# Kernel tuning notes

Hardware: AMD Instinct MI355X
Metric: run time of the kernel (lower is better)

## Reference

```python
import jax, jax.numpy as jnp
import numpy as np

N, E, D = 50000, 800000, 128
BN_EPS = 1e-5
COORDS_WEIGHT = 1.0


def _p(key, shape, scale=0.05):
    return (jax.random.normal(key, shape, dtype=jnp.float32) * scale)


def setup_inputs() -> dict:
    key = jax.random.key(0)
    ks = jax.random.split(key, 16)
    inp = {
        "h": jax.random.normal(ks[0], (N, D), dtype=jnp.float32),
        "coord": jax.random.normal(ks[1], (N, 3), dtype=jnp.float32),
        "edge_index": jax.random.randint(ks[2], (2, E), 0, N, dtype=jnp.int32),
        # edge_mlp: Linear(2D+1 -> D), BN, ReLU, Linear(D -> D), BN, ReLU
        "e_w1": _p(ks[3], (D, 2 * D + 1)), "e_b1": jnp.zeros((D,), jnp.float32),
        "e_g1": jnp.ones((D,), jnp.float32), "e_be1": jnp.zeros((D,), jnp.float32),
        "e_w2": _p(ks[4], (D, D)), "e_b2": jnp.zeros((D,), jnp.float32),
        "e_g2": jnp.ones((D,), jnp.float32), "e_be2": jnp.zeros((D,), jnp.float32),
        # node_mlp: Linear(D + D -> D), BN, ReLU, Linear(D -> D)
        "n_w1": _p(ks[5], (D, 2 * D)), "n_b1": jnp.zeros((D,), jnp.float32),
        "n_g1": jnp.ones((D,), jnp.float32), "n_be1": jnp.zeros((D,), jnp.float32),
        "n_w2": _p(ks[6], (D, D)), "n_b2": jnp.zeros((D,), jnp.float32),
        # coord_mlp: Linear(D -> D), BN, ReLU, Linear(D -> 1, bias=False, tiny init)
        "c_w1": _p(ks[7], (D, D)), "c_b1": jnp.zeros((D,), jnp.float32),
        "c_g1": jnp.ones((D,), jnp.float32), "c_be1": jnp.zeros((D,), jnp.float32),
        "c_w2": _p(ks[8], (1, D), scale=0.001),
    }
    return inp


def _bn(x, g, b):
    # BatchNorm1d in training mode: biased batch stats over dim 0
    m = jnp.mean(x, axis=0)
    v = jnp.var(x, axis=0)
    return (x - m) * jax.lax.rsqrt(v + BN_EPS) * g + b


def _segment_mean(data, seg, num_segments):
    s = jax.ops.segment_sum(data, seg, num_segments=num_segments)
    c = jax.ops.segment_sum(jnp.ones((data.shape[0], 1), data.dtype), seg,
                            num_segments=num_segments)
    return s / jnp.maximum(c, 1.0)


def reference(h, coord, edge_index,
              e_w1, e_b1, e_g1, e_be1, e_w2, e_b2, e_g2, e_be2,
              n_w1, n_b1, n_g1, n_be1, n_w2, n_b2,
              c_w1, c_b1, c_g1, c_be1, c_w2):
    row, col = edge_index[0], edge_index[1]
    # coord2radial
    coord_diff = coord[row] - coord[col]                      # [E,3]
    radial = jnp.sum(coord_diff ** 2, axis=1, keepdims=True)  # [E,1]
    # edge_model
    e_in = jnp.concatenate([h[row], h[col], radial], axis=1)  # [E, 2D+1]
    x = jax.nn.relu(_bn(e_in @ e_w1.T + e_b1, e_g1, e_be1))
    edge_feat = jax.nn.relu(_bn(x @ e_w2.T + e_b2, e_g2, e_be2))  # [E,D]
    # coord_model
    y = jax.nn.relu(_bn(edge_feat @ c_w1.T + c_b1, c_g1, c_be1))
    scale = y @ c_w2.T                                        # [E,1]
    trans = jnp.clip(coord_diff * scale, -100.0, 100.0)
    coord_out = coord + _segment_mean(trans, row, coord.shape[0]) * COORDS_WEIGHT
    # node_model
    agg = _segment_mean(edge_feat, row, h.shape[0])           # [N,D]
    n_in = jnp.concatenate([h, agg], axis=1)                  # [N,2D]
    z = jax.nn.relu(_bn(n_in @ n_w1.T + n_b1, n_g1, n_be1))
    h_out = h + (z @ n_w2.T + n_b2)                           # recurrent residual
    return (h_out, coord_out)
```

## Files before the change

### kernel.cpp

```cpp
#include <hip/hip_runtime.h>

#define Nn 50000
#define En 800000
#define NSLOT 64
#define MGRID 384

typedef __attribute__((ext_vector_type(8))) short short8;
typedef __attribute__((ext_vector_type(4))) float f32x4;

union U8 { uint4 u4; unsigned short us[8]; unsigned int ui[4]; short8 s8; };

static __device__ __forceinline__ float bf2f(unsigned int lo16) {
  return __uint_as_float(lo16 << 16);
}
static __device__ __forceinline__ unsigned short f2bf(float f) {
  unsigned int x = __float_as_uint(f);
  return (unsigned short)((x + 0x7FFFu + ((x >> 16) & 1u)) >> 16);
}
static __device__ __forceinline__ unsigned int f2bf2(float a, float b) {
  unsigned int r;
  asm("v_cvt_pk_bf16_f32 %0, %1, %2" : "=v"(r) : "v"(a), "v"(b));
  return r;
}


__global__ __launch_bounds__(256) void k_prep_h(const float* __restrict__ h,
                                                unsigned short* __restrict__ nodeA) {
  int idx = blockIdx.x * 256 + threadIdx.x;
  if (idx >= Nn * 128) return;
  int n = idx >> 7, k = idx & 127;
  nodeA[(size_t)n * 256 + k] = f2bf(h[idx]);
}

__global__ __launch_bounds__(256) void k_prep_w(const float* __restrict__ src,
                                                unsigned short* __restrict__ dst, int Ksrc,
                                                int koff, int kshift, int total) {
  int idx = blockIdx.x * 256 + threadIdx.x;
  if (idx >= total) return;
  int n = idx >> kshift;
  int k = idx & ((1 << kshift) - 1);
  dst[idx] = f2bf(src[n * Ksrc + koff + k]);
}

__global__ void k_wlast(const float* __restrict__ e_w1, float* __restrict__ wlast) {
  int t = threadIdx.x;
  if (t < 128) wlast[t] = e_w1[t * 257 + 256];
}


__global__ __launch_bounds__(256) void k_count(const int* __restrict__ row, int* __restrict__ cnt) {
  int e = blockIdx.x * 256 + threadIdx.x;
  atomicAdd(&cnt[row[e]], 1);
}

__global__ __launch_bounds__(256) void k_fill(const int* __restrict__ row,
                                              const int* __restrict__ col,
                                              int* __restrict__ cursor,
                                              unsigned short* __restrict__ rowS,
                                              unsigned short* __restrict__ colS) {
  int e = blockIdx.x * 256 + threadIdx.x;
  int r = row[e];
  int pos = atomicAdd(&cursor[r], 1);
  rowS[pos] = (unsigned short)r;
  colS[pos] = (unsigned short)col[e];
}

__global__ __launch_bounds__(1024) void k_scan(const int* __restrict__ cnt, int* __restrict__ start,
                                               int* __restrict__ cursor, int n) {
  __shared__ int wsum[16];
  __shared__ int carry;
  int tid = threadIdx.x, lane = tid & 63, wid = tid >> 6;
  if (tid == 0) carry = 0;
  __syncthreads();
  for (int base = 0; base < n; base += 1024) {
    int i = base + tid;
    int v = (i < n) ? cnt[i] : 0;
    int x = v;
#pragma unroll
    for (int d = 1; d < 64; d <<= 1) {
      int y = __shfl_up(x, d, 64);
      if (lane >= d) x += y;
    }
    if (lane == 63) wsum[wid] = x;
    __syncthreads();
    if (wid == 0) {
      int s = (lane < 16) ? wsum[lane] : 0;
#pragma unroll
      for (int d = 1; d < 16; d <<= 1) {
        int y = __shfl_up(s, d, 64);
        if (lane >= d) s += y;
      }
      if (lane < 16) wsum[lane] = s;
    }
    __syncthreads();
    int c0 = carry;
    int waveoff = (wid > 0) ? wsum[wid - 1] : 0;
    int incl = c0 + waveoff + x;
    if (i < n) {
      start[i] = incl - v;
      cursor[i] = incl - v;
    }
    __syncthreads();
    if (tid == 1023) carry = incl;
    __syncthreads();
  }
}


__global__ void k_fin(const float* __restrict__ statS, const float* __restrict__ statQ,
                      const float* __restrict__ g, const float* __restrict__ be, float invR,
                      float* __restrict__ bnS, float* __restrict__ bnSh) {
  int c = threadIdx.x;
  if (c >= 128) return;
  float s = 0.f, q = 0.f;
  for (int k = 0; k < NSLOT; ++k) {
    s += statS[k * 128 + c];
    q += statQ[k * 128 + c];
  }
  float mean = s * invR;
  float var = fmaxf(q * invR - mean * mean, 0.f);
  float rs = rsqrtf(var + 1e-5f);
  float sc = g[c] * rs;
  bnS[c] = sc;
  bnSh[c] = be[c] - mean * sc;
}

template <int KSTEPS, bool BN_A, bool STATS, bool FP32OUT, bool STORE>
__global__ __launch_bounds__(256) void k_gemmW(
    const unsigned short* __restrict__ A, int Astride,
    const unsigned short* __restrict__ W, const float* __restrict__ bias,
    const float* __restrict__ bnS, const float* __restrict__ bnSh,
    unsigned short* __restrict__ outb, float* __restrict__ statS, float* __restrict__ statQ,
    const float* __restrict__ hres, float* __restrict__ outf, int R) {
  constexpr int K = KSTEPS * 32;
  constexpr int WST = K + 8;
  constexpr int SEGS = K / 8;
  __shared__ __align__(16) unsigned short smem[128 * WST];
  __shared__ float ssum[4][128], ssq[4][128];
  int tid = threadIdx.x;
  int w = tid >> 6, lane = tid & 63, m = lane & 15, kq = lane >> 4;
  int rbase = blockIdx.x * 128;
#pragma unroll
  for (int it = 0; it < SEGS / 2; ++it) {
    int idx = it * 256 + tid;
    int n = idx / SEGS, seg = idx % SEGS;
    uint4 v = *(const uint4*)(W + (size_t)n * K + seg * 8);
    *(uint4*)(smem + n * WST + seg * 8) = v;
  }
  __syncthreads();
  int row0 = rbase + w * 32 + m;
  int rc0 = min(row0, R - 1);
  int rc1 = min(row0 + 16, R - 1);
  f32x4 acc[2][8];
#pragma unroll
  for (int rt = 0; rt < 2; ++rt)
#pragma unroll
    for (int c = 0; c < 8; ++c) acc[rt][c] = (f32x4){0.f, 0.f, 0.f, 0.f};
#pragma unroll
  for (int ks = 0; ks < KSTEPS; ++ks) {
    int k0 = ks * 32 + kq * 8;
    U8 ua0, ua1;
    ua0.u4 = *(const uint4*)(A + (size_t)rc0 * Astride + k0);
    ua1.u4 = *(const uint4*)(A + (size_t)rc1 * Astride + k0);
    if (BN_A) {
      const float4* sp = (const float4*)(bnS + k0);
      const float4* hp = (const float4*)(bnSh + k0);
      float4 s0 = sp[0], s1 = sp[1], h0 = hp[0], h1 = hp[1];
      float sv[8] = {s0.x, s0.y, s0.z, s0.w, s1.x, s1.y, s1.z, s1.w};
      float hv[8] = {h0.x, h0.y, h0.z, h0.w, h1.x, h1.y, h1.z, h1.w};
      U8 pa, pb;
#pragma unroll
      for (int jj = 0; jj < 4; ++jj) {
        float a0 = fmaxf(bf2f(ua0.us[2 * jj]) * sv[2 * jj] + hv[2 * jj], 0.f);
        float a1 = fmaxf(bf2f(ua0.us[2 * jj + 1]) * sv[2 * jj + 1] + hv[2 * jj + 1], 0.f);
        float b0 = fmaxf(bf2f(ua1.us[2 * jj]) * sv[2 * jj] + hv[2 * jj], 0.f);
        float b1 = fmaxf(bf2f(ua1.us[2 * jj + 1]) * sv[2 * jj + 1] + hv[2 * jj + 1], 0.f);
        pa.ui[jj] = f2bf2(a0, a1);
        pb.ui[jj] = f2bf2(b0, b1);
      }
      ua0 = pa;
      ua1 = pb;
    }
#pragma unroll
    for (int c = 0; c < 8; ++c) {
      U8 ub;
      ub.u4 = *(const uint4*)(smem + (c * 16 + m) * WST + k0);
      acc[0][c] = __builtin_amdgcn_mfma_f32_16x16x32_bf16(ua0.s8, ub.s8, acc[0][c], 0, 0, 0);
      acc[1][c] = __builtin_amdgcn_mfma_f32_16x16x32_bf16(ua1.s8, ub.s8, acc[1][c], 0, 0, 0);
    }
  }
  if constexpr (FP32OUT) {
#pragma unroll
    for (int rt = 0; rt < 2; ++rt)
#pragma unroll
      for (int c = 0; c < 8; ++c) {
        int n = c * 16 + m;
        float bn_ = bias[n];
#pragma unroll
        for (int j = 0; j < 4; ++j) {
          int rr = rbase + w * 32 + rt * 16 + kq * 4 + j;
          if (rr < R) {
            size_t o = (size_t)rr * 128 + n;
            outf[o] = acc[rt][c][j] + bn_ + hres[o];
          }
        }
      }
  } else {
    if constexpr (STORE) __syncthreads();
    unsigned short* tile = smem;
#pragma unroll
    for (int c = 0; c < 8; ++c) {
      int n = c * 16 + m;
      float bn_ = bias ? bias[n] : 0.f;
      float s = 0.f, q = 0.f;
#pragma unroll
      for (int rt = 0; rt < 2; ++rt)
#pragma unroll
        for (int j = 0; j < 4; ++j) {
          int lr = w * 32 + rt * 16 + kq * 4 + j;
          float v = acc[rt][c][j] + bn_;
          if (STORE) tile[lr * 136 + n] = f2bf(v);
          if (STATS) {
            float sv = (rbase + lr < R) ? v : 0.f;
            s += sv;
            q = fmaf(sv, sv, q);
          }
        }
      if (STATS) {
        s += __shfl_xor(s, 16, 64); s += __shfl_xor(s, 32, 64);
        q += __shfl_xor(q, 16, 64); q += __shfl_xor(q, 32, 64);
        if (kq == 0) { ssum[w][n] = s; ssq[w][n] = q; }
      }
    }
    if constexpr (STORE) {
      __syncthreads();
      const uint4* tl = (const uint4*)tile;
#pragma unroll
      for (int u = 0; u < 8; ++u) {
        int idx = u * 256 + tid;
        int rr = idx >> 4, seg = idx & 15;
        if (rbase + rr < R)
          *(uint4*)(outb + (size_t)(rbase + rr) * 128 + seg * 8) = tl[rr * 17 + seg];
      }
    }
    if (STATS) {
      __syncthreads();
      if (tid < 128) {
        float s = ssum[0][tid] + ssum[1][tid] + ssum[2][tid] + ssum[3][tid];
        float q = ssq[0][tid] + ssq[1][tid] + ssq[2][tid] + ssq[3][tid];
        int slot = blockIdx.x & (NSLOT - 1);
        atomicAdd(&statS[slot * 128 + tid], s);
        atomicAdd(&statQ[slot * 128 + tid], q);
      }
    }
  }
}

__global__ __launch_bounds__(256) void k_stats1(
    const unsigned short* __restrict__ hWr, const unsigned short* __restrict__ hWc,
    const float* __restrict__ coord, const unsigned short* __restrict__ rowS,
    const unsigned short* __restrict__ colS, const float* __restrict__ wlast,
    float* __restrict__ radS, float* __restrict__ statS, float* __restrict__ statQ,
    int per_wave) {
  int tid = threadIdx.x, lane = tid & 63;
  int wid = blockIdx.x * 4 + (tid >> 6);
  int e0 = wid * per_wave;
  int e1 = min(e0 + per_wave, En);
  int c2 = lane * 2;
  float wl0 = wlast[c2], wl1 = wlast[c2 + 1];
  float s0 = 0.f, s1 = 0.f, q0 = 0.f, q1 = 0.f;
  for (int e = e0; e < e1; e += 2) {
    int ra = rowS[e], ca = colS[e];
    int rb = rowS[e + 1], cb = colS[e + 1];
    float ax = coord[ra * 3 + 0] - coord[ca * 3 + 0];
    float ay = coord[ra * 3 + 1] - coord[ca * 3 + 1];
    float az = coord[ra * 3 + 2] - coord[ca * 3 + 2];
    float bx = coord[rb * 3 + 0] - coord[cb * 3 + 0];
    float by = coord[rb * 3 + 1] - coord[cb * 3 + 1];
    float bz = coord[rb * 3 + 2] - coord[cb * 3 + 2];
    float rada = ax * ax + ay * ay + az * az;
    float radb = bx * bx + by * by + bz * bz;
    if (lane == 0) {
      radS[e] = rada;
      radS[e + 1] = radb;
    }
    unsigned int uar = *(const unsigned int*)(hWr + (size_t)ra * 128 + c2);
    unsigned int uac = *(const unsigned int*)(hWc + (size_t)ca * 128 + c2);
    unsigned int ubr = *(const unsigned int*)(hWr + (size_t)rb * 128 + c2);
    unsigned int ubc = *(const unsigned int*)(hWc + (size_t)cb * 128 + c2);
    float va0 = bf2f(uar & 0xFFFFu) + bf2f(uac & 0xFFFFu) + rada * wl0;
    float va1 = bf2f(uar >> 16) + bf2f(uac >> 16) + rada * wl1;
    float vb0 = bf2f(ubr & 0xFFFFu) + bf2f(ubc & 0xFFFFu) + radb * wl0;
    float vb1 = bf2f(ubr >> 16) + bf2f(ubc >> 16) + radb * wl1;
    s0 += va0 + vb0;
    s1 += va1 + vb1;
    q0 = fmaf(va0, va0, q0); q0 = fmaf(vb0, vb0, q0);
    q1 = fmaf(va1, va1, q1); q1 = fmaf(vb1, vb1, q1);
  }
  int slot = wid & (NSLOT - 1);
  atomicAdd(&statS[slot * 128 + c2], s0);
  atomicAdd(&statS[slot * 128 + c2 + 1], s1);
  atomicAdd(&statQ[slot * 128 + c2], q0);
  atomicAdd(&statQ[slot * 128 + c2 + 1], q1);
}

__global__ __launch_bounds__(256) void k_egemm2(
    const unsigned short* __restrict__ hWr, const unsigned short* __restrict__ hWc,
    const float* __restrict__ radS, const unsigned short* __restrict__ rowS,
    const unsigned short* __restrict__ colS, const unsigned short* __restrict__ W,
    const float* __restrict__ bias, const float* __restrict__ wlast,
    const float* __restrict__ bnS1, const float* __restrict__ bnSh1,
    unsigned short* __restrict__ outb, float* __restrict__ statS, float* __restrict__ statQ) {
  constexpr int WST = 136;
  __shared__ __align__(16) unsigned short smem[128 * WST];
  __shared__ float ssum[4][128], ssq[4][128];
  int tid = threadIdx.x;
  int w = tid >> 6, lane = tid & 63, m = lane & 15, kq = lane >> 4;
  int rbase = blockIdx.x * 128;
#pragma unroll
  for (int it = 0; it < 8; ++it) {
    int idx = it * 256 + tid;
    int n = idx >> 4, seg = idx & 15;
    uint4 v = *(const uint4*)(W + (size_t)n * 128 + seg * 8);
    *(uint4*)(smem + n * WST + seg * 8) = v;
  }
  int rc0 = rbase + w * 32 + m, rc1 = rc0 + 16;
  int r0 = rowS[rc0], c0 = colS[rc0];
  int r1 = rowS[rc1], c1 = colS[rc1];
  float rad0 = radS[rc0], rad1 = radS[rc1];
  __syncthreads();
  f32x4 acc[2][8];
#pragma unroll
  for (int rt = 0; rt < 2; ++rt)
#pragma unroll
    for (int c = 0; c < 8; ++c) acc[rt][c] = (f32x4){0.f, 0.f, 0.f, 0.f};
#pragma unroll
  for (int ks = 0; ks < 4; ++ks) {
    int k0 = ks * 32 + kq * 8;
    U8 a0r, a0c, a1r, a1c;
    a0r.u4 = *(const uint4*)(hWr + (size_t)r0 * 128 + k0);
    a0c.u4 = *(const uint4*)(hWc + (size_t)c0 * 128 + k0);
    a1r.u4 = *(const uint4*)(hWr + (size_t)r1 * 128 + k0);
    a1c.u4 = *(const uint4*)(hWc + (size_t)c1 * 128 + k0);
    const float4* wp = (const float4*)(wlast + k0);
    const float4* sp = (const float4*)(bnS1 + k0);
    const float4* hp = (const float4*)(bnSh1 + k0);
    float4 w0 = wp[0], w1 = wp[1], sA = sp[0], sB = sp[1], hA = hp[0], hB = hp[1];
    float wv[8] = {w0.x, w0.y, w0.z, w0.w, w1.x, w1.y, w1.z, w1.w};
    float sv[8] = {sA.x, sA.y, sA.z, sA.w, sB.x, sB.y, sB.z, sB.w};
    float hv[8] = {hA.x, hA.y, hA.z, hA.w, hB.x, hB.y, hB.z, hB.w};
    U8 ua0, ua1;
#pragma unroll
    for (int jj = 0; jj < 4; ++jj) {
      int j0 = 2 * jj, j1 = 2 * jj + 1;
      float v0a = bf2f(a0r.us[j0]) + bf2f(a0c.us[j0]) + rad0 * wv[j0];
      float v0b = bf2f(a0r.us[j1]) + bf2f(a0c.us[j1]) + rad0 * wv[j1];
      float v1a = bf2f(a1r.us[j0]) + bf2f(a1c.us[j0]) + rad1 * wv[j0];
      float v1b = bf2f(a1r.us[j1]) + bf2f(a1c.us[j1]) + rad1 * wv[j1];
      v0a = fmaxf(v0a * sv[j0] + hv[j0], 0.f);
      v0b = fmaxf(v0b * sv[j1] + hv[j1], 0.f);
      v1a = fmaxf(v1a * sv[j0] + hv[j0], 0.f);
      v1b = fmaxf(v1b * sv[j1] + hv[j1], 0.f);
      ua0.ui[jj] = f2bf2(v0a, v0b);
      ua1.ui[jj] = f2bf2(v1a, v1b);
    }
#pragma unroll
    for (int c = 0; c < 8; ++c) {
      U8 ub;
      ub.u4 = *(const uint4*)(smem + (c * 16 + m) * WST + k0);
      acc[0][c] = __builtin_amdgcn_mfma_f32_16x16x32_bf16(ua0.s8, ub.s8, acc[0][c], 0, 0, 0);
      acc[1][c] = __builtin_amdgcn_mfma_f32_16x16x32_bf16(ua1.s8, ub.s8, acc[1][c], 0, 0, 0);
    }
  }
  __syncthreads();
  unsigned short* tile = smem;
#pragma unroll
  for (int c = 0; c < 8; ++c) {
    int n = c * 16 + m;
    float bn_ = bias[n];
    float s = 0.f, q = 0.f;
#pragma unroll
    for (int rt = 0; rt < 2; ++rt)
#pragma unroll
      for (int j = 0; j < 4; ++j) {
        int lr = w * 32 + rt * 16 + kq * 4 + j;
        float v = acc[rt][c][j] + bn_;
        tile[lr * 136 + n] = f2bf(v);
        s += v;
        q = fmaf(v, v, q);
      }
    s += __shfl_xor(s, 16, 64); s += __shfl_xor(s, 32, 64);
    q += __shfl_xor(q, 16, 64); q += __shfl_xor(q, 32, 64);
    if (kq == 0) { ssum[w][n] = s; ssq[w][n] = q; }
  }
  __syncthreads();
  const uint4* tl = (const uint4*)tile;
#pragma unroll
  for (int u = 0; u < 8; ++u) {
    int idx = u * 256 + tid;
    int rr = idx >> 4, seg = idx & 15;
    *(uint4*)(outb + (size_t)(rbase + rr) * 128 + seg * 8) = tl[rr * 17 + seg];
  }
  if (tid < 128) {
    float s = ssum[0][tid] + ssum[1][tid] + ssum[2][tid] + ssum[3][tid];
    float q = ssq[0][tid] + ssq[1][tid] + ssq[2][tid] + ssq[3][tid];
    int slot = blockIdx.x & (NSLOT - 1);
    atomicAdd(&statS[slot * 128 + tid], s);
    atomicAdd(&statQ[slot * 128 + tid], q);
  }
}

__global__ __launch_bounds__(256) void k_agg(const unsigned short* __restrict__ t,
                                             const int* __restrict__ start,
                                             const int* __restrict__ cnt,
                                             const float* __restrict__ bnS,
                                             const float* __restrict__ bnSh,
                                             unsigned short* __restrict__ nodeA) {
  int tid = threadIdx.x;
  int lane = tid & 63;
  int n = blockIdx.x * 4 + (tid >> 6);
  if (n >= Nn) return;
  int deg = cnt[n], off = start[n];
  int c2 = lane * 2;
  float s0 = bnS[c2], s1 = bnS[c2 + 1], h0 = bnSh[c2], h1 = bnSh[c2 + 1];
  float a0 = 0.f, a1 = 0.f;
  const unsigned short* p = t + (size_t)off * 128 + c2;
  for (int j = 0; j < deg; ++j) {
    unsigned int u = *(const unsigned int*)(p + (size_t)j * 128);
    a0 += fmaxf(bf2f(u & 0xFFFFu) * s0 + h0, 0.f);
    a1 += fmaxf(bf2f(u >> 16) * s1 + h1, 0.f);
  }
  float inv = 1.f / fmaxf((float)deg, 1.f);
  unsigned int o = (unsigned)f2bf(a0 * inv) | ((unsigned)f2bf(a1 * inv) << 16);
  *(unsigned int*)(nodeA + (size_t)n * 256 + 128 + c2) = o;
}

__global__ __launch_bounds__(256) void k_moment(
    const unsigned short* __restrict__ t,
    const float* __restrict__ bnS2, const float* __restrict__ bnSh2,
    float* __restrict__ Mpart, float* __restrict__ SyG) {
  constexpr int WST = 136;
  __shared__ __align__(16) unsigned short yT[128 * WST];
  __shared__ float s2L[128], h2L[128];
  int tid = threadIdx.x;
  int w = tid >> 6, lane = tid & 63, m = lane & 15, kq = lane >> 4;
  if (tid < 128) { s2L[tid] = bnS2[tid]; h2L[tid] = bnSh2[tid]; }
  f32x4 acc[2][8];
#pragma unroll
  for (int rt = 0; rt < 2; ++rt)
#pragma unroll
    for (int c = 0; c < 8; ++c) acc[rt][c] = (f32x4){0.f, 0.f, 0.f, 0.f};
  float sy[32];
#pragma unroll
  for (int i = 0; i < 32; ++i) sy[i] = 0.f;
  for (int tile = blockIdx.x; tile < En / 128; tile += MGRID) {
    __syncthreads();
    int e0 = tile * 128 + lane * 2;
    U8 ra[4], rb[4];
#pragma unroll
    for (int q = 0; q < 4; ++q) {
      ra[q].u4 = *(const uint4*)(t + (size_t)e0 * 128 + w * 32 + q * 8);
      rb[q].u4 = *(const uint4*)(t + (size_t)(e0 + 1) * 128 + w * 32 + q * 8);
    }
#pragma unroll
    for (int q = 0; q < 4; ++q)
#pragma unroll
      for (int i = 0; i < 8; ++i) {
        int c = w * 32 + q * 8 + i;
        float s = s2L[c], h = h2L[c];
        float ya = fmaxf(bf2f(ra[q].us[i]) * s + h, 0.f);
        float yb = fmaxf(bf2f(rb[q].us[i]) * s + h, 0.f);
        sy[q * 8 + i] += ya + yb;
        *(unsigned int*)(yT + c * WST + lane * 2) = f2bf2(ya, yb);
      }
    __syncthreads();
#pragma unroll
    for (int ks = 0; ks < 4; ++ks) {
      int k0 = ks * 32 + kq * 8;
      U8 a0, a1;
      a0.u4 = *(const uint4*)(yT + (w * 32 + m) * WST + k0);
      a1.u4 = *(const uint4*)(yT + (w * 32 + 16 + m) * WST + k0);
#pragma unroll
      for (int c = 0; c < 8; ++c) {
        U8 ub;
        ub.u4 = *(const uint4*)(yT + (c * 16 + m) * WST + k0);
        acc[0][c] = __builtin_amdgcn_mfma_f32_16x16x32_bf16(a0.s8, ub.s8, acc[0][c], 0, 0, 0);
        acc[1][c] = __builtin_amdgcn_mfma_f32_16x16x32_bf16(a1.s8, ub.s8, acc[1][c], 0, 0, 0);
      }
    }
  }
  size_t mb = (size_t)blockIdx.x * 16384;
#pragma unroll
  for (int rt = 0; rt < 2; ++rt)
#pragma unroll
    for (int c = 0; c < 8; ++c)
#pragma unroll
      for (int j = 0; j < 4; ++j)
        Mpart[mb + (size_t)(w * 32 + rt * 16 + kq * 4 + j) * 128 + c * 16 + m] = acc[rt][c][j];
#pragma unroll
  for (int i = 0; i < 32; ++i) {
    float s = sy[i];
#pragma unroll
    for (int d = 1; d < 64; d <<= 1) s += __shfl_xor(s, d, 64);
    if (lane == 0) atomicAdd(&SyG[w * 32 + i], s);
  }
}

__global__ __launch_bounds__(256) void k_msum(const float* __restrict__ Mpart,
                                              float* __restrict__ Mg) {
  __shared__ float red[4][64];
  int tid = threadIdx.x;
  int e = blockIdx.x * 64 + (tid & 63);
  int pq = tid >> 6;
  float s = 0.f;
  for (int k = pq * (MGRID / 4); k < (pq + 1) * (MGRID / 4); ++k)
    s += Mpart[(size_t)k * 16384 + e];
  red[pq][tid & 63] = s;
  __syncthreads();
  if (tid < 64) Mg[e] = red[0][tid] + red[1][tid] + red[2][tid] + red[3][tid];
}

__global__ __launch_bounds__(128) void k_fin3(
    const float* __restrict__ Mg, const float* __restrict__ Sy,
    const float* __restrict__ w1, const float* __restrict__ g,
    const float* __restrict__ be, float invE,
    float* __restrict__ bnS3, float* __restrict__ bnSh3) {
  __shared__ float sW[128];
  __shared__ float r2[4];
  int c = blockIdx.x, j = threadIdx.x;
  sW[j] = w1[c * 128 + j];
  __syncthreads();
  float a0 = 0.f, a1 = 0.f, a2 = 0.f, a3 = 0.f;
  for (int i = 0; i < 128; i += 4) {
    a0 = fmaf(sW[i], Mg[i * 128 + j], a0);
    a1 = fmaf(sW[i + 1], Mg[(i + 1) * 128 + j], a1);
    a2 = fmaf(sW[i + 2], Mg[(i + 2) * 128 + j], a2);
    a3 = fmaf(sW[i + 3], Mg[(i + 3) * 128 + j], a3);
  }
  float q = sW[j] * ((a0 + a1) + (a2 + a3));
  float dm = sW[j] * Sy[j];
#pragma unroll
  for (int d = 1; d < 64; d <<= 1) {
    q += __shfl_xor(q, d, 64);
    dm += __shfl_xor(dm, d, 64);
  }
  int wv = j >> 6;
  if ((j & 63) == 0) { r2[wv * 2] = q; r2[wv * 2 + 1] = dm; }
  __syncthreads();
  if (j == 0) {
    float quad = r2[0] + r2[2];
    float dmt = r2[1] + r2[3];
    float Eu = dmt * invE;
    float var = fmaxf(quad * invE - Eu * Eu, 0.f);
    float S = g[c] * rsqrtf(var + 1e-5f);
    bnS3[c] = S;
    bnSh3[c] = be[c] - Eu * S;
  }
}

__global__ __launch_bounds__(256) void k_cgemm(
    const unsigned short* __restrict__ A,
    const unsigned short* __restrict__ W,
    const float* __restrict__ bnS2, const float* __restrict__ bnSh2,
    const float* __restrict__ bnS3, const float* __restrict__ bnSh3,
    const float* __restrict__ cw2, float* __restrict__ scaleE) {
  constexpr int WST = 136;
  __shared__ __align__(16) unsigned short smem[128 * WST];
  int tid = threadIdx.x;
  int w = tid >> 6, lane = tid & 63, m = lane & 15, kq = lane >> 4;
  int rbase = blockIdx.x * 128;
#pragma unroll
  for (int it = 0; it < 8; ++it) {
    int idx = it * 256 + tid;
    int n = idx >> 4, seg = idx & 15;
    *(uint4*)(smem + n * WST + seg * 8) = *(const uint4*)(W + (size_t)n * 128 + seg * 8);
  }
  __syncthreads();
  int rc0 = rbase + w * 32 + m, rc1 = rc0 + 16;
  f32x4 acc[2][8];
#pragma unroll
  for (int rt = 0; rt < 2; ++rt)
#pragma unroll
    for (int c = 0; c < 8; ++c) acc[rt][c] = (f32x4){0.f, 0.f, 0.f, 0.f};
#pragma unroll
  for (int ks = 0; ks < 4; ++ks) {
    int k0 = ks * 32 + kq * 8;
    U8 ua0, ua1;
    ua0.u4 = *(const uint4*)(A + (size_t)rc0 * 128 + k0);
    ua1.u4 = *(const uint4*)(A + (size_t)rc1 * 128 + k0);
    const float4* sp = (const float4*)(bnS2 + k0);
    const float4* hp = (const float4*)(bnSh2 + k0);
    float4 s0 = sp[0], s1 = sp[1], h0 = hp[0], h1 = hp[1];
    float sv[8] = {s0.x, s0.y, s0.z, s0.w, s1.x, s1.y, s1.z, s1.w};
    float hv[8] = {h0.x, h0.y, h0.z, h0.w, h1.x, h1.y, h1.z, h1.w};
    U8 pa, pb;
#pragma unroll
    for (int jj = 0; jj < 4; ++jj) {
      float v0a = fmaxf(bf2f(ua0.us[2 * jj]) * sv[2 * jj] + hv[2 * jj], 0.f);
      float v0b = fmaxf(bf2f(ua0.us[2 * jj + 1]) * sv[2 * jj + 1] + hv[2 * jj + 1], 0.f);
      float v1a = fmaxf(bf2f(ua1.us[2 * jj]) * sv[2 * jj] + hv[2 * jj], 0.f);
      float v1b = fmaxf(bf2f(ua1.us[2 * jj + 1]) * sv[2 * jj + 1] + hv[2 * jj + 1], 0.f);
      pa.ui[jj] = f2bf2(v0a, v0b);
      pb.ui[jj] = f2bf2(v1a, v1b);
    }
#pragma unroll
    for (int c = 0; c < 8; ++c) {
      U8 ub;
      ub.u4 = *(const uint4*)(smem + (c * 16 + m) * WST + k0);
      acc[0][c] = __builtin_amdgcn_mfma_f32_16x16x32_bf16(pa.s8, ub.s8, acc[0][c], 0, 0, 0);
      acc[1][c] = __builtin_amdgcn_mfma_f32_16x16x32_bf16(pb.s8, ub.s8, acc[1][c], 0, 0, 0);
    }
  }
  float s3v[8], h3v[8], wv[8];
#pragma unroll
  for (int c = 0; c < 8; ++c) {
    int n = c * 16 + m;
    s3v[c] = bnS3[n];
    h3v[c] = bnSh3[n];
    wv[c] = cw2[n];
  }
  float p0[4] = {0.f, 0.f, 0.f, 0.f}, p1[4] = {0.f, 0.f, 0.f, 0.f};
#pragma unroll
  for (int c = 0; c < 8; ++c)
#pragma unroll
    for (int j = 0; j < 4; ++j) {
      p0[j] += fmaxf(acc[0][c][j] * s3v[c] + h3v[c], 0.f) * wv[c];
      p1[j] += fmaxf(acc[1][c][j] * s3v[c] + h3v[c], 0.f) * wv[c];
    }
#pragma unroll
  for (int j = 0; j < 4; ++j)
#pragma unroll
    for (int d = 1; d < 16; d <<= 1) {
      p0[j] += __shfl_xor(p0[j], d, 64);
      p1[j] += __shfl_xor(p1[j], d, 64);
    }
  if (m == 0) {
    int r0 = rbase + w * 32 + kq * 4;
    *(float4*)(scaleE + r0) = make_float4(p0[0], p0[1], p0[2], p0[3]);
    *(float4*)(scaleE + r0 + 16) = make_float4(p1[0], p1[1], p1[2], p1[3]);
  }
}

__global__ __launch_bounds__(256) void k_coord(const float* __restrict__ coord,
                                               const unsigned short* __restrict__ colS,
                                               const int* __restrict__ start,
                                               const int* __restrict__ cnt,
                                               const float* __restrict__ scaleE,
                                               float* __restrict__ cout) {
  int tid = threadIdx.x;
  int lane = tid & 63;
  int n = blockIdx.x * 4 + (tid >> 6);
  if (n >= Nn) return;
  int deg = cnt[n], off = start[n];
  float cx0 = coord[n * 3 + 0], cy0 = coord[n * 3 + 1], cz0 = coord[n * 3 + 2];
  float ax = 0.f, ay = 0.f, az = 0.f;
  for (int j = lane; j < deg; j += 64) {
    int e = off + j;
    int c = colS[e];
    float s = scaleE[e];
    float tx = (cx0 - coord[c * 3 + 0]) * s;
    float ty = (cy0 - coord[c * 3 + 1]) * s;
    float tz = (cz0 - coord[c * 3 + 2]) * s;
    ax += fminf(fmaxf(tx, -100.f), 100.f);
    ay += fminf(fmaxf(ty, -100.f), 100.f);
    az += fminf(fmaxf(tz, -100.f), 100.f);
  }
#pragma unroll
  for (int d = 32; d; d >>= 1) {
    ax += __shfl_xor(ax, d, 64);
    ay += __shfl_xor(ay, d, 64);
    az += __shfl_xor(az, d, 64);
  }
  if (lane == 0) {
    float inv = 1.f / fmaxf((float)deg, 1.f);
    cout[n * 3 + 0] = cx0 + ax * inv;
    cout[n * 3 + 1] = cy0 + ay * inv;
    cout[n * 3 + 2] = cz0 + az * inv;
  }
}


extern "C" void kernel_launch(void* const* d_in, const int* in_sizes, int n_in, void* d_out,
                              int out_size, void* d_ws, size_t ws_size, hipStream_t stream) {
  (void)in_sizes; (void)n_in; (void)out_size; (void)ws_size;
  const float* h = (const float*)d_in[0];
  const float* coord = (const float*)d_in[1];
  const int* eidx = (const int*)d_in[2];
  const int* row = eidx;
  const int* col = eidx + En;
  const float* e_w1 = (const float*)d_in[3];
  const float* e_b1 = (const float*)d_in[4];
  const float* e_g1 = (const float*)d_in[5];
  const float* e_be1 = (const float*)d_in[6];
  const float* e_w2 = (const float*)d_in[7];
  const float* e_b2 = (const float*)d_in[8];
  const float* e_g2 = (const float*)d_in[9];
  const float* e_be2 = (const float*)d_in[10];
  const float* n_w1 = (const float*)d_in[11];
  const float* n_b1 = (const float*)d_in[12];
  const float* n_g1 = (const float*)d_in[13];
  const float* n_be1 = (const float*)d_in[14];
  const float* n_w2 = (const float*)d_in[15];
  const float* n_b2 = (const float*)d_in[16];
  const float* c_w1 = (const float*)d_in[17];
  const float* c_b1 = (const float*)d_in[18];
  (void)c_b1;
  const float* c_g1 = (const float*)d_in[19];
  const float* c_be1 = (const float*)d_in[20];
  const float* c_w2 = (const float*)d_in[21];

  char* base = (char*)d_ws;
  size_t off = 0;
  auto alloc = [&](size_t bytes) -> void* {
    void* p = base + off;
    off = (off + bytes + 255) & ~(size_t)255;
    return p;
  };
  unsigned short* t = (unsigned short*)alloc((size_t)En * 128 * 2);
  unsigned short* nodeA = (unsigned short*)alloc((size_t)Nn * 256 * 2);
  unsigned short* hWr = (unsigned short*)alloc((size_t)Nn * 128 * 2);
  unsigned short* hWc = (unsigned short*)alloc((size_t)Nn * 128 * 2);
  float* scaleE = (float*)alloc((size_t)En * 4);
  float* radS = scaleE;
  unsigned short* rowS = (unsigned short*)alloc((size_t)En * 2);
  unsigned short* colS = (unsigned short*)alloc((size_t)En * 2);
  int* cnt = (int*)alloc((size_t)Nn * 4);
  int* startp = (int*)alloc((size_t)Nn * 4);
  int* cursor = (int*)alloc((size_t)Nn * 4);
  float* statS = (float*)alloc(4 * NSLOT * 128 * 4);
  float* statQ = (float*)alloc(4 * NSLOT * 128 * 4);
  float* bnS = (float*)alloc(4 * 128 * 4);
  float* bnSh = (float*)alloc(4 * 128 * 4);
  unsigned short* w1a = (unsigned short*)alloc(128 * 128 * 2);
  unsigned short* w1b = (unsigned short*)alloc(128 * 128 * 2);
  unsigned short* w2b = (unsigned short*)alloc(128 * 128 * 2);
  unsigned short* c1b = (unsigned short*)alloc(128 * 128 * 2);
  unsigned short* n1b = (unsigned short*)alloc(128 * 256 * 2);
  unsigned short* n2b = (unsigned short*)alloc(128 * 128 * 2);
  float* wlast = (float*)alloc(128 * 4);
  float* Mpart = (float*)hWr;
  float* Mg = scaleE;
  float* SyG = scaleE + 16384;

  hipMemsetAsync(cnt, 0, (size_t)Nn * 4, stream);
  hipMemsetAsync(statS, 0, 4 * NSLOT * 128 * 4, stream);
  hipMemsetAsync(statQ, 0, 4 * NSLOT * 128 * 4, stream);

  k_prep_h<<<(Nn * 128 + 255) / 256, 256, 0, stream>>>(h, nodeA);
  k_prep_w<<<(128 * 128 + 255) / 256, 256, 0, stream>>>(e_w1, w1a, 257, 0, 7, 128 * 128);
  k_prep_w<<<(128 * 128 + 255) / 256, 256, 0, stream>>>(e_w1, w1b, 257, 128, 7, 128 * 128);
  k_prep_w<<<(128 * 128 + 255) / 256, 256, 0, stream>>>(e_w2, w2b, 128, 0, 7, 128 * 128);
  k_prep_w<<<(128 * 128 + 255) / 256, 256, 0, stream>>>(c_w1, c1b, 128, 0, 7, 128 * 128);
  k_prep_w<<<(128 * 256 + 255) / 256, 256, 0, stream>>>(n_w1, n1b, 256, 0, 8, 128 * 256);
  k_prep_w<<<(128 * 128 + 255) / 256, 256, 0, stream>>>(n_w2, n2b, 128, 0, 7, 128 * 128);
  k_wlast<<<1, 128, 0, stream>>>(e_w1, wlast);

  k_count<<<En / 256, 256, 0, stream>>>(row, cnt);
  k_scan<<<1, 1024, 0, stream>>>(cnt, startp, cursor, Nn);
  k_fill<<<En / 256, 256, 0, stream>>>(row, col, cursor, rowS, colS);

  const int gridN = (Nn + 127) / 128;
  k_gemmW<4, false, false, false, true><<<gridN, 256, 0, stream>>>(
      nodeA, 256, w1a, e_b1, nullptr, nullptr, hWr, nullptr, nullptr, nullptr, nullptr, Nn);
  k_gemmW<4, false, false, false, true><<<gridN, 256, 0, stream>>>(
      nodeA, 256, w1b, nullptr, nullptr, nullptr, hWc, nullptr, nullptr, nullptr, nullptr, Nn);

  const int per_wave = ((En / 2 + 5119) / 5120) * 2;
  k_stats1<<<1280, 256, 0, stream>>>(hWr, hWc, coord, rowS, colS, wlast, radS,
                                     statS + 0 * NSLOT * 128, statQ + 0 * NSLOT * 128, per_wave);
  k_fin<<<1, 128, 0, stream>>>(statS + 0 * NSLOT * 128, statQ + 0 * NSLOT * 128, e_g1, e_be1,
                               1.f / En, bnS + 0, bnSh + 0);

  k_egemm2<<<En / 128, 256, 0, stream>>>(hWr, hWc, radS, rowS, colS, w2b, e_b2, wlast, bnS + 0,
                                         bnSh + 0, t, statS + 1 * NSLOT * 128,
                                         statQ + 1 * NSLOT * 128);
  k_fin<<<1, 128, 0, stream>>>(statS + 1 * NSLOT * 128, statQ + 1 * NSLOT * 128, e_g2, e_be2,
                               1.f / En, bnS + 128, bnSh + 128);

  k_agg<<<(Nn + 3) / 4, 256, 0, stream>>>(t, startp, cnt, bnS + 128, bnSh + 128, nodeA);

  hipMemsetAsync(SyG, 0, 128 * 4, stream);
  k_moment<<<MGRID, 256, 0, stream>>>(t, bnS + 128, bnSh + 128, Mpart, SyG);
  k_msum<<<256, 256, 0, stream>>>(Mpart, Mg);
  k_fin3<<<128, 128, 0, stream>>>(Mg, SyG, c_w1, c_g1, c_be1, 1.f / En, bnS + 256, bnSh + 256);

  k_cgemm<<<En / 128, 256, 0, stream>>>(t, c1b, bnS + 128, bnSh + 128, bnS + 256, bnSh + 256,
                                        c_w2, scaleE);

  float* hout = (float*)d_out;
  float* cout = hout + (size_t)Nn * 128;
  k_coord<<<(Nn + 3) / 4, 256, 0, stream>>>(coord, colS, startp, cnt, scaleE, cout);

  k_gemmW<8, false, true, false, true><<<gridN, 256, 0, stream>>>(
      nodeA, 256, n1b, n_b1, nullptr, nullptr, t, statS + 3 * NSLOT * 128,
      statQ + 3 * NSLOT * 128, nullptr, nullptr, Nn);
  k_fin<<<1, 128, 0, stream>>>(statS + 3 * NSLOT * 128, statQ + 3 * NSLOT * 128, n_g1, n_be1,
                               1.f / Nn, bnS + 384, bnSh + 384);
  k_gemmW<4, true, false, true, true><<<gridN, 256, 0, stream>>>(
      t, 128, n2b, n_b2, bnS + 384, bnSh + 384, nullptr, nullptr, nullptr, h, hout, Nn);
}
```

Measured before the change: 917.7 us.

## Double the k_moment block to 8 waves and prefetch next tile into registers

The second-moment (Gram matrix) kernel now runs 512 threads per block, so each wave owns 16 feature rows instead of 32 and keeps half the accumulators. The BN scale and shift values are hoisted into registers, and the next tile's bf16 inputs are loaded into registers while the current tile is transformed and multiplied. This is meant to hide global-load latency and raise wave occupancy, at the cost of more registers for the prefetch buffers and a larger block.

```diff
diff --git a/kernel.cpp b/kernel.cpp
--- a/kernel.cpp
+++ b/kernel.cpp
@@ -435,74 +435,85 @@
   *(unsigned int*)(nodeA + (size_t)n * 256 + 128 + c2) = o;
 }
 
-__global__ __launch_bounds__(256) void k_moment(
+__global__ __launch_bounds__(512) void k_moment(
     const unsigned short* __restrict__ t,
     const float* __restrict__ bnS2, const float* __restrict__ bnSh2,
     float* __restrict__ Mpart, float* __restrict__ SyG) {
   constexpr int WST = 136;
+  constexpr int NT = En / 128;
   __shared__ __align__(16) unsigned short yT[128 * WST];
   __shared__ float s2L[128], h2L[128];
   int tid = threadIdx.x;
   int w = tid >> 6, lane = tid & 63, m = lane & 15, kq = lane >> 4;
   if (tid < 128) { s2L[tid] = bnS2[tid]; h2L[tid] = bnSh2[tid]; }
-  f32x4 acc[2][8];
-#pragma unroll
-  for (int rt = 0; rt < 2; ++rt)
-#pragma unroll
-    for (int c = 0; c < 8; ++c) acc[rt][c] = (f32x4){0.f, 0.f, 0.f, 0.f};
-  float sy[32];
-#pragma unroll
-  for (int i = 0; i < 32; ++i) sy[i] = 0.f;
-  for (int tile = blockIdx.x; tile < En / 128; tile += MGRID) {
+  __syncthreads();
+  float sA[16], hA[16];
+#pragma unroll
+  for (int c = 0; c < 16; ++c) { sA[c] = s2L[w * 16 + c]; hA[c] = h2L[w * 16 + c]; }
+  f32x4 acc[8];
+#pragma unroll
+  for (int c = 0; c < 8; ++c) acc[c] = (f32x4){0.f, 0.f, 0.f, 0.f};
+  float sy[16];
+#pragma unroll
+  for (int c = 0; c < 16; ++c) sy[c] = 0.f;
+  int tile = blockIdx.x;
+  U8 cura0, cura1, curb0, curb1, nxta0, nxta1, nxtb0, nxtb1;
+  {
+    const unsigned short* p = t + ((size_t)tile * 128 + lane * 2) * 128 + w * 16;
+    cura0.u4 = *(const uint4*)(p);
+    cura1.u4 = *(const uint4*)(p + 8);
+    curb0.u4 = *(const uint4*)(p + 128);
+    curb1.u4 = *(const uint4*)(p + 136);
+  }
+  while (tile < NT) {
+    int nxt = tile + MGRID;
+    unsigned int pk[16];
+#pragma unroll
+    for (int c = 0; c < 16; ++c) {
+      float ya = fmaxf(bf2f((c < 8) ? cura0.us[c & 7] : cura1.us[c & 7]) * sA[c] + hA[c], 0.f);
+      float yb = fmaxf(bf2f((c < 8) ? curb0.us[c & 7] : curb1.us[c & 7]) * sA[c] + hA[c], 0.f);
+      sy[c] += ya + yb;
+      pk[c] = f2bf2(ya, yb);
+    }
+    if (nxt < NT) {
+      const unsigned short* p = t + ((size_t)nxt * 128 + lane * 2) * 128 + w * 16;
+      nxta0.u4 = *(const uint4*)(p);
+      nxta1.u4 = *(const uint4*)(p + 8);
+      nxtb0.u4 = *(const uint4*)(p + 128);
+      nxtb1.u4 = *(const uint4*)(p + 136);
+    }
     __syncthreads();
-    int e0 = tile * 128 + lane * 2;
-    U8 ra[4], rb[4];
-#pragma unroll
-    for (int q = 0; q < 4; ++q) {
-      ra[q].u4 = *(const uint4*)(t + (size_t)e0 * 128 + w * 32 + q * 8);
-      rb[q].u4 = *(const uint4*)(t + (size_t)(e0 + 1) * 128 + w * 32 + q * 8);
-    }
-#pragma unroll
-    for (int q = 0; q < 4; ++q)
-#pragma unroll
-      for (int i = 0; i < 8; ++i) {
-        int c = w * 32 + q * 8 + i;
-        float s = s2L[c], h = h2L[c];
-        float ya = fmaxf(bf2f(ra[q].us[i]) * s + h, 0.f);
-        float yb = fmaxf(bf2f(rb[q].us[i]) * s + h, 0.f);
-        sy[q * 8 + i] += ya + yb;
-        *(unsigned int*)(yT + c * WST + lane * 2) = f2bf2(ya, yb);
-      }
+#pragma unroll
+    for (int c = 0; c < 16; ++c)
+      *(unsigned int*)(yT + (w * 16 + c) * WST + lane * 2) = pk[c];
     __syncthreads();
 #pragma unroll
     for (int ks = 0; ks < 4; ++ks) {
       int k0 = ks * 32 + kq * 8;
-      U8 a0, a1;
-      a0.u4 = *(const uint4*)(yT + (w * 32 + m) * WST + k0);
-      a1.u4 = *(const uint4*)(yT + (w * 32 + 16 + m) * WST + k0);
+      U8 a;
+      a.u4 = *(const uint4*)(yT + (w * 16 + m) * WST + k0);
 #pragma unroll
       for (int c = 0; c < 8; ++c) {
-        U8 ub;
-        ub.u4 = *(const uint4*)(yT + (c * 16 + m) * WST + k0);
-        acc[0][c] = __builtin_amdgcn_mfma_f32_16x16x32_bf16(a0.s8, ub.s8, acc[0][c], 0, 0, 0);
-        acc[1][c] = __builtin_amdgcn_mfma_f32_16x16x32_bf16(a1.s8, ub.s8, acc[1][c], 0, 0, 0);
+        U8 b;
+        b.u4 = *(const uint4*)(yT + (c * 16 + m) * WST + k0);
+        acc[c] = __builtin_amdgcn_mfma_f32_16x16x32_bf16(a.s8, b.s8, acc[c], 0, 0, 0);
       }
     }
+    cura0 = nxta0; cura1 = nxta1; curb0 = nxtb0; curb1 = nxtb1;
+    tile = nxt;
   }
   size_t mb = (size_t)blockIdx.x * 16384;
 #pragma unroll
-  for (int rt = 0; rt < 2; ++rt)
-#pragma unroll
-    for (int c = 0; c < 8; ++c)
-#pragma unroll
-      for (int j = 0; j < 4; ++j)
-        Mpart[mb + (size_t)(w * 32 + rt * 16 + kq * 4 + j) * 128 + c * 16 + m] = acc[rt][c][j];
-#pragma unroll
-  for (int i = 0; i < 32; ++i) {
-    float s = sy[i];
+  for (int c = 0; c < 8; ++c)
+#pragma unroll
+    for (int j = 0; j < 4; ++j)
+      Mpart[mb + (size_t)(w * 16 + kq * 4 + j) * 128 + c * 16 + m] = acc[c][j];
+#pragma unroll
+  for (int c = 0; c < 16; ++c) {
+    float s = sy[c];
 #pragma unroll
     for (int d = 1; d < 64; d <<= 1) s += __shfl_xor(s, d, 64);
-    if (lane == 0) atomicAdd(&SyG[w * 32 + i], s);
+    if (lane == 0) atomicAdd(&SyG[w * 16 + c], s);
   }
 }
 
@@ -780,7 +791,7 @@
   k_agg<<<(Nn + 3) / 4, 256, 0, stream>>>(t, startp, cnt, bnS + 128, bnSh + 128, nodeA);
 
   hipMemsetAsync(SyG, 0, 128 * 4, stream);
-  k_moment<<<MGRID, 256, 0, stream>>>(t, bnS + 128, bnSh + 128, Mpart, SyG);
+  k_moment<<<MGRID, 512, 0, stream>>>(t, bnS + 128, bnSh + 128, Mpart, SyG);
   k_msum<<<256, 256, 0, stream>>>(Mpart, Mg);
   k_fin3<<<128, 128, 0, stream>>>(Mg, SyG, c_w1, c_g1, c_be1, 1.f / En, bnS + 256, bnSh + 256);
 
```

Result: no change. 915.6 us (-0.2%).
